# Kernel optimization log

Measured on AMD Instinct MI355X. Metric: run time of the kernel, lower is better.

The kernel has to match this reference:

```python
import jax, jax.numpy as jnp
import numpy as np

HEADS = 16
MAX_SEQ_LEN = 1024
ALPHA = 1.0


def setup_inputs() -> dict:
    key = jax.random.key(0)
    ks = jax.random.split(key, 16)
    b, n, dim = 2, 1024, 1024
    s = 0.02
    x = jax.random.normal(ks[0], (b, n, dim), jnp.float32)
    Wq = jax.random.normal(ks[1], (dim, dim), jnp.float32) * s
    Wk = jax.random.normal(ks[2], (dim, dim), jnp.float32) * s
    Wv = jax.random.normal(ks[3], (dim, dim), jnp.float32) * s
    Wo = jax.random.normal(ks[4], (dim, dim), jnp.float32) * s
    E_idx = jax.random.normal(ks[5], (MAX_SEQ_LEN, HEADS), jnp.float32) * s
    # padding_idx=0 rows zero-initialized (as in torch nn.Embedding(padding_idx=0))
    E_bar = (jax.random.normal(ks[6], (17, HEADS), jnp.float32) * s).at[0].set(0.0)
    E_pos = (jax.random.normal(ks[7], (96, HEADS), jnp.float32) * s).at[0].set(0.0)
    E_oct = (jax.random.normal(ks[8], (25, HEADS), jnp.float32) * s).at[0].set(0.0)
    E_semi = (jax.random.normal(ks[9], (13, HEADS), jnp.float32) * s).at[0].set(0.0)
    # structure matrices: raw values in [0, table_size-2]; forward adds +1
    bar = jax.random.randint(ks[10], (b, n, n), 0, 16, dtype=jnp.int32)
    position = jax.random.randint(ks[11], (b, n, n), 0, 95, dtype=jnp.int32)
    octave = jax.random.randint(ks[12], (b, n, n), 0, 24, dtype=jnp.int32)
    semitone = jax.random.randint(ks[13], (b, n, n), 0, 12, dtype=jnp.int32)
    return {"x": x, "Wq": Wq, "Wk": Wk, "Wv": Wv, "Wo": Wo,
            "E_idx": E_idx, "E_bar": E_bar, "E_pos": E_pos,
            "E_oct": E_oct, "E_semi": E_semi,
            "bar": bar, "position": position, "octave": octave, "semitone": semitone}


def reference(x, Wq, Wk, Wv, Wo, E_idx, E_bar, E_pos, E_oct, E_semi,
              bar, position, octave, semitone):
    b, n, dim = x.shape
    h = HEADS
    d = dim // h

    def split_heads(t):  # (b,n,dim) -> (b,h,n,d)
        return t.reshape(b, n, h, d).transpose(0, 2, 1, 3)

    q = split_heads(x @ Wq.T)
    k = split_heads(x @ Wk.T)
    v = split_heads(x @ Wv.T)

    qk = jnp.einsum('bhid,bhjd->bhij', q, k)

    # relative index bias: (1,h,n,n)
    rel_pos = jnp.clip(jnp.arange(n)[:, None] - jnp.arange(n)[None, :], 0, MAX_SEQ_LEN - 1)
    srel = E_idx[rel_pos].transpose(2, 0, 1)[None]

    # structure biases: embedding lookups -> (b,h,n,n)
    s_time = (E_bar[bar + 1] + E_pos[position + 1]).transpose(0, 3, 1, 2)
    s_pitch = (E_oct[octave + 1] + E_semi[semitone + 1]).transpose(0, 3, 1, 2)

    dots = (qk + ALPHA * (srel + s_time + s_pitch)) / jnp.sqrt(jnp.float32(d))

    causal_mask = jnp.triu(jnp.ones((n, n), dtype=bool), k=1)
    mask_value = -jnp.finfo(dots.dtype).max
    dots = jnp.where(causal_mask, mask_value, dots)

    attn = jax.nn.softmax(dots, axis=-1)  # dropout=0 at eval
    out = jnp.einsum('bhij,bhjd->bhid', attn, v)
    out = out.transpose(0, 2, 1, 3).reshape(b, n, dim)
    return out @ Wo.T
```

## Files before the change

kernel.cpp:

```cpp
#include <hip/hip_runtime.h>
#include <cstdint>
#include <math.h>

typedef __attribute__((ext_vector_type(8))) short short8;
typedef __attribute__((ext_vector_type(4))) float f32x4;

#define LOG2E 1.44269504088896340736f

static __device__ __forceinline__ float bf2f(unsigned short u) {
    union { unsigned int i; float f; } v; v.i = ((unsigned int)u) << 16; return v.f;
}
static __device__ __forceinline__ unsigned short f2bf(float f) {
    union { float f; unsigned int i; } v; v.f = f;
    unsigned int r = v.i + 0x7FFF + ((v.i >> 16) & 1);
    return (unsigned short)(r >> 16);
}

__global__ __launch_bounds__(256) void k_convert(
    const float* __restrict__ x, const float* __restrict__ wq,
    const float* __restrict__ wk, const float* __restrict__ wv,
    const float* __restrict__ wo, unsigned short* __restrict__ dst) {
    long t = (long)blockIdx.x * 256 + threadIdx.x;
    long base = t * 4;
    const long NX = 2097152, NW = 1048576;
    const float* src; long off;
    if (base < NX)            { src = x;  off = base; }
    else if (base < NX + NW)  { src = wq; off = base - NX; }
    else if (base < NX + 2*NW){ src = wk; off = base - NX - NW; }
    else if (base < NX + 3*NW){ src = wv; off = base - NX - 2*NW; }
    else                      { src = wo; off = base - NX - 3*NW; }
    float4 v = *(const float4*)(src + off);
    ushort4 o;
    o.x = f2bf(v.x); o.y = f2bf(v.y); o.z = f2bf(v.z); o.w = f2bf(v.w);
    *(ushort4*)(dst + base) = o;
}

__global__ __launch_bounds__(256) void k_bias(
    const float* __restrict__ Eidx, const float* __restrict__ Ebar,
    const float* __restrict__ Epos, const float* __restrict__ Eoct,
    const float* __restrict__ Esemi,
    const int* __restrict__ barm, const int* __restrict__ posm,
    const int* __restrict__ octm, const int* __restrict__ semim,
    unsigned short* __restrict__ biasg) {
    int fid = blockIdx.x;
    int b = (fid >= 544) ? 1 : 0;
    int f = fid - b * 544;
    int ti, tj;
    if (f >= 480) { int rr = f - 480; ti = 60 + (rr >> 4); tj = rr & 15; }
    else {
        int g = (int)(0.5f * (sqrtf(1.0f + 2.0f * (float)f) - 1.0f));
        while (2 * (g + 1) * (g + 2) <= f) g++;
        while (2 * g * (g + 1) > f) g--;
        int rr = f - 2 * g * (g + 1);
        int q = rr / (g + 1);
        ti = g * 4 + q;
        tj = rr - q * (g + 1);
    }
    int i0 = ti * 16, j0 = tj * 64;

    __shared__ float2 t2[8 * 233];
    __shared__ int    pk[16 * 65];

    int t = threadIdx.x;
    int rel_lo = i0 - j0 - 63; if (rel_lo < 0) rel_lo = 0;

    for (int idx = t; idx < 231 * 8; idx += 256) {
        int s = idx >> 3, h2 = idx & 7;
        float va, vb;
        if (s < 80) {
            int src = rel_lo + s; if (src > 1023) src = 1023;
            va = Eidx[src * 16 + h2]; vb = Eidx[src * 16 + h2 + 8];
        } else if (s < 97)  { va = Ebar[(s - 80) * 16 + h2];  vb = Ebar[(s - 80) * 16 + h2 + 8]; }
        else if (s < 193)   { va = Epos[(s - 97) * 16 + h2];  vb = Epos[(s - 97) * 16 + h2 + 8]; }
        else if (s < 218)   { va = Eoct[(s - 193) * 16 + h2]; vb = Eoct[(s - 193) * 16 + h2 + 8]; }
        else                { va = Esemi[(s - 218) * 16 + h2]; vb = Esemi[(s - 218) * 16 + h2 + 8]; }
        t2[h2 * 233 + s] = make_float2(va, vb);
    }
    #pragma unroll
    for (int cc = 0; cc < 4; cc++) {
        int cell = t + cc * 256;
        int i = i0 + (cell >> 6), j = j0 + (cell & 63);
        long ij = ((long)b << 20) + ((long)i << 10) + j;
        int v = (barm[ij] + 1) | ((posm[ij] + 1) << 5) |
                ((octm[ij] + 1) << 12) | ((semim[ij] + 1) << 17);
        pk[(cell >> 6) * 65 + (cell & 63)] = v;
    }
    __syncthreads();

    int r = t & 15, h2 = (t >> 4) & 7, ah = t >> 7;
    int i = i0 + r;
    int base_rel = i - j0 - rel_lo;
    const float2* T = &t2[h2 * 233];
    long frag = (r >> 2) * 256 + (r & 3) * 4;
    unsigned short* dstL = biasg + ((((long)(b * 16 + h2)     * 64 + ti) * 16 + tj) << 10) + frag;
    unsigned short* dstH = biasg + ((((long)(b * 16 + h2 + 8) * 64 + ti) * 16 + tj) << 10) + frag;
    #pragma unroll 4
    for (int aa = 0; aa < 8; aa++) {
        int a = ah * 8 + aa;
        ushort4 ovL, ovH;
        #pragma unroll
        for (int jj = 0; jj < 4; jj++) {
            int col = a + 16 * jj;
            int p = pk[r * 65 + col];
            int sr = base_rel - col; if (sr < 0) sr = 0;
            float2 v0 = T[sr];
            float2 v1 = T[80  + (p & 31)];
            float2 v2 = T[97  + ((p >> 5)  & 127)];
            float2 v3 = T[193 + ((p >> 12) & 31)];
            float2 v4 = T[218 + ((p >> 17) & 15)];
            float xL = v0.x + v1.x + v2.x + v3.x + v4.x;
            float xH = v0.y + v1.y + v2.y + v3.y + v4.y;
            ((unsigned short*)&ovL)[jj] = f2bf(xL * 0.125f);
            ((unsigned short*)&ovH)[jj] = f2bf(xH * 0.125f);
        }
        *(ushort4*)(dstL + a * 16) = ovL;
        *(ushort4*)(dstH + a * 16) = ovH;
    }
}

__global__ __launch_bounds__(256) void k_gemm(
    const unsigned short* __restrict__ A,
    const unsigned short* __restrict__ B0, const unsigned short* __restrict__ B1,
    const unsigned short* __restrict__ B2,
    unsigned short* __restrict__ qd, unsigned short* __restrict__ kd,
    unsigned short* __restrict__ vtd, float* __restrict__ outf, int mode) {
    __shared__ unsigned short As[128 * 64];
    __shared__ unsigned short Bs[128 * 64];
    int md = (mode < 0) ? (int)blockIdx.z : mode;
    const unsigned short* B = (md == 1) ? B1 : (md == 2) ? B2 : B0;
    int m0 = blockIdx.x * 128, n0 = blockIdx.y * 128;
    int t = threadIdx.x;
    int w = t >> 6, lane = t & 63, g = lane >> 4, c = lane & 15;
    int wr = w >> 1, wc = w & 1;
    const int K = 1024;
    f32x4 zero = {0.f, 0.f, 0.f, 0.f};
    f32x4 acc[4][4];
    #pragma unroll
    for (int m = 0; m < 4; m++)
        #pragma unroll
        for (int n = 0; n < 4; n++) acc[m][n] = zero;

    int srow = w * 8 + (lane >> 3);
    int scol = (lane & 7) * 8;
    for (int k0 = 0; k0 < K; k0 += 64) {
        __syncthreads();
        #pragma unroll
        for (int q = 0; q < 4; q++) {
            int row = q * 32 + srow;
            __builtin_amdgcn_global_load_lds(
                (const __attribute__((address_space(1))) unsigned int*)(A + (long)(m0 + row) * K + k0 + scol),
                (__attribute__((address_space(3))) unsigned int*)&As[(q * 32 + w * 8) * 64],
                16, 0, 0);
            __builtin_amdgcn_global_load_lds(
                (const __attribute__((address_space(1))) unsigned int*)(B + (long)(n0 + row) * K + k0 + scol),
                (__attribute__((address_space(3))) unsigned int*)&Bs[(q * 32 + w * 8) * 64],
                16, 0, 0);
        }
        __syncthreads();
        #pragma unroll
        for (int kk = 0; kk < 2; kk++) {
            short8 a[4], bb[4];
            #pragma unroll
            for (int m = 0; m < 4; m++)
                a[m] = *(const short8*)&As[(wr * 64 + m * 16 + c) * 64 + kk * 32 + g * 8];
            #pragma unroll
            for (int n = 0; n < 4; n++)
                bb[n] = *(const short8*)&Bs[(wc * 64 + n * 16 + c) * 64 + kk * 32 + g * 8];
            #pragma unroll
            for (int m = 0; m < 4; m++)
                #pragma unroll
                for (int n = 0; n < 4; n++)
                    acc[m][n] = __builtin_amdgcn_mfma_f32_16x16x32_bf16(a[m], bb[n], acc[m][n], 0, 0, 0);
        }
    }

    if (md <= 1) {
        unsigned short* dst = (md == 0) ? qd : kd;
        float scale = (md == 0) ? 0.125f : 1.0f;
        #pragma unroll
        for (int m = 0; m < 4; m++) {
            #pragma unroll
            for (int r = 0; r < 4; r++) {
                int mm = m0 + wr * 64 + m * 16 + g * 4 + r;
                int bb2 = mm >> 10, ii = mm & 1023;
                #pragma unroll
                for (int n = 0; n < 4; n++) {
                    int nn = n0 + wc * 64 + n * 16 + c;
                    int hh = nn >> 6, dd = nn & 63;
                    dst[(((long)(bb2 * 16 + hh) << 10) + ii) * 64 + dd] = f2bf(acc[m][n][r] * scale);
                }
            }
        }
    } else if (md == 2) {
        #pragma unroll
        for (int m = 0; m < 4; m++) {
            int mm0 = m0 + wr * 64 + m * 16 + g * 4;
            int bb2 = mm0 >> 10, ii = mm0 & 1023;
            #pragma unroll
            for (int n = 0; n < 4; n++) {
                int nn = n0 + wc * 64 + n * 16 + c;
                int hh = nn >> 6, dd = nn & 63;
                ushort4 pkv;
                pkv.x = f2bf(acc[m][n][0]); pkv.y = f2bf(acc[m][n][1]);
                pkv.z = f2bf(acc[m][n][2]); pkv.w = f2bf(acc[m][n][3]);
                *(ushort4*)&vtd[(((long)(bb2 * 16 + hh) << 6) + dd) * 1024 + ii] = pkv;
            }
        }
    } else {
        #pragma unroll
        for (int m = 0; m < 4; m++) {
            #pragma unroll
            for (int r = 0; r < 4; r++) {
                long mm = m0 + wr * 64 + m * 16 + g * 4 + r;
                #pragma unroll
                for (int n = 0; n < 4; n++) {
                    int nn = n0 + wc * 64 + n * 16 + c;
                    outf[mm * 1024 + nn] = acc[m][n][r];
                }
            }
        }
    }
}

__global__ __launch_bounds__(256) void k_attn(
    const unsigned short* __restrict__ Qs, const unsigned short* __restrict__ Ks,
    const unsigned short* __restrict__ VTs, const unsigned short* __restrict__ biasg,
    unsigned short* __restrict__ Os) {
    __shared__ char smem[4 * 5632];
    int bid = blockIdx.x;
    int it = 63 - (bid >> 5);
    int bh = bid & 31;
    int b = bh >> 4, h = bh & 15;
    int w = threadIdx.x >> 6;
    int lane = threadIdx.x & 63;
    int g = lane >> 4, c = lane & 15;
    int i0 = it * 16;

    char* wbase = smem + w * 5632;
    unsigned short* p_lds = (unsigned short*)wbase;

    long plane = ((long)bh) << 16;
    const unsigned short* Qp = Qs + plane;
    const unsigned short* Kp = Ks + plane;
    const unsigned short* Vp = VTs + plane;
    const unsigned short* Bt = biasg + (((long)bh * 64 + it) << 14);

    short8 q0 = *(const short8*)(Qp + (long)(i0 + c) * 64 + g * 8);
    short8 q1 = *(const short8*)(Qp + (long)(i0 + c) * 64 + 32 + g * 8);

    f32x4 zero = {0.f, 0.f, 0.f, 0.f};
    f32x4 o[4]; o[0] = zero; o[1] = zero; o[2] = zero; o[3] = zero;
    float l[4] = {0.f, 0.f, 0.f, 0.f};

    int nj = (it >> 2) + 1;
    for (int jt = w; jt < nj; jt += 4) {
        int j0 = jt * 64;
        f32x4 s[4]; s[0] = zero; s[1] = zero; s[2] = zero; s[3] = zero;
        #pragma unroll
        for (int jj = 0; jj < 4; jj++) {
            const unsigned short* kr = Kp + (long)(j0 + jj * 16 + c) * 64 + g * 8;
            short8 ka = *(const short8*)(kr);
            short8 kb = *(const short8*)(kr + 32);
            s[jj] = __builtin_amdgcn_mfma_f32_16x16x32_bf16(q0, ka, s[jj], 0, 0, 0);
            s[jj] = __builtin_amdgcn_mfma_f32_16x16x32_bf16(q1, kb, s[jj], 0, 0, 0);
        }
        const unsigned short* bp = Bt + (jt << 10) + lane * 16;
        short8 bv0 = *(const short8*)(bp);
        short8 bv1 = *(const short8*)(bp + 8);
        #pragma unroll
        for (int r = 0; r < 4; r++) {
            #pragma unroll
            for (int jj = 0; jj < 4; jj++) {
                int idx = r * 4 + jj;
                float bb = (idx < 8) ? bf2f((unsigned short)bv0[idx])
                                     : bf2f((unsigned short)bv1[idx - 8]);
                s[jj][r] += bb;
            }
        }
        if (jt == nj - 1) {
            #pragma unroll
            for (int r = 0; r < 4; r++) {
                int i = i0 + g * 4 + r;
                #pragma unroll
                for (int jj = 0; jj < 4; jj++) {
                    if (j0 + jj * 16 + c > i) s[jj][r] = -1e9f;
                }
            }
        }
        #pragma unroll
        for (int r = 0; r < 4; r++) {
            #pragma unroll
            for (int jj = 0; jj < 4; jj++) {
                float p = exp2f(__builtin_fmaf(s[jj][r], LOG2E, -8.0f * LOG2E));
                l[r] += p;
                union { float f; unsigned int u; } pu; pu.f = p;
                p_lds[(g * 4 + r) * 72 + c + 16 * jj] = (unsigned short)(pu.u >> 16);
            }
        }
        short8 pa0 = *(const short8*)&p_lds[c * 72 + g * 8];
        short8 pa1 = *(const short8*)&p_lds[c * 72 + 32 + g * 8];
        #pragma unroll
        for (int dd = 0; dd < 4; dd++) {
            const unsigned short* vb = Vp + (long)(dd * 16 + c) * 1024 + j0 + g * 8;
            short8 v0 = *(const short8*)(vb);
            short8 v1 = *(const short8*)(vb + 32);
            o[dd] = __builtin_amdgcn_mfma_f32_16x16x32_bf16(pa0, v0, o[dd], 0, 0, 0);
            o[dd] = __builtin_amdgcn_mfma_f32_16x16x32_bf16(pa1, v1, o[dd], 0, 0, 0);
        }
    }
    float* oc = (float*)wbase;
    float* lc = (float*)(wbase + 4352);
    #pragma unroll
    for (int dd = 0; dd < 4; dd++)
        #pragma unroll
        for (int r = 0; r < 4; r++)
            oc[lane * 17 + dd * 4 + r] = o[dd][r];
    #pragma unroll
    for (int r = 0; r < 4; r++) lc[lane * 5 + r] = l[r];
    __syncthreads();

    if (w == 0) {
        float linv[4];
        #pragma unroll
        for (int r = 0; r < 4; r++) {
            float lv = 0.f;
            #pragma unroll
            for (int ww = 0; ww < 4; ww++)
                lv += ((const float*)(smem + ww * 5632 + 4352))[lane * 5 + r];
            lv += __shfl_xor(lv, 1); lv += __shfl_xor(lv, 2);
            lv += __shfl_xor(lv, 4); lv += __shfl_xor(lv, 8);
            linv[r] = 1.0f / lv;
        }
        #pragma unroll
        for (int r = 0; r < 4; r++) {
            int i = i0 + g * 4 + r;
            unsigned short* op = Os + ((long)(b * 1024 + i)) * 1024 + h * 64;
            #pragma unroll
            for (int dd = 0; dd < 4; dd++) {
                float ov = 0.f;
                #pragma unroll
                for (int ww = 0; ww < 4; ww++)
                    ov += ((const float*)(smem + ww * 5632))[lane * 17 + dd * 4 + r];
                op[dd * 16 + c] = f2bf(ov * linv[r]);
            }
        }
    }
}

extern "C" void kernel_launch(void* const* d_in, const int* in_sizes, int n_in,
                              void* d_out, int out_size, void* d_ws, size_t ws_size,
                              hipStream_t stream) {
    const float* x     = (const float*)d_in[0];
    const float* Wq    = (const float*)d_in[1];
    const float* Wk    = (const float*)d_in[2];
    const float* Wv    = (const float*)d_in[3];
    const float* Wo    = (const float*)d_in[4];
    const float* Eidx  = (const float*)d_in[5];
    const float* Ebar  = (const float*)d_in[6];
    const float* Epos  = (const float*)d_in[7];
    const float* Eoct  = (const float*)d_in[8];
    const float* Esemi = (const float*)d_in[9];
    const int* barm    = (const int*)d_in[10];
    const int* posm    = (const int*)d_in[11];
    const int* octm    = (const int*)d_in[12];
    const int* semim   = (const int*)d_in[13];
    float* outf = (float*)d_out;

    unsigned short* w = (unsigned short*)d_ws;
    unsigned short* XB   = w;
    unsigned short* WQB  = w + 2097152;
    unsigned short* WKB  = w + 3145728;
    unsigned short* WVB  = w + 4194304;
    unsigned short* WOB  = w + 5242880;
    unsigned short* QS   = w + 6291456;
    unsigned short* KS   = w + 8388608;
    unsigned short* VTS  = w + 10485760;
    unsigned short* OS   = w + 12582912;
    unsigned short* BIAS = w + 14680064;

    k_convert<<<6144, 256, 0, stream>>>(x, Wq, Wk, Wv, Wo, w);
    k_bias<<<1088, 256, 0, stream>>>(Eidx, Ebar, Epos, Eoct, Esemi,
                                     barm, posm, octm, semim, BIAS);
    k_gemm<<<dim3(16, 8, 3), 256, 0, stream>>>(XB, WQB, WKB, WVB,
                                               QS, KS, VTS, nullptr, -1);
    k_attn<<<2048, 256, 0, stream>>>(QS, KS, VTS, BIAS, OS);
    k_gemm<<<dim3(16, 8, 1), 256, 0, stream>>>(OS, WOB, WOB, WOB,
                                               QS, KS, VTS, outf, 3);
}
```

Measured before the change: 119.9 us.

## Widen attention key tile to 128 and split epilogue across waves

Each attention loop iteration now covers 128 keys instead of 64. All K fragments and bias vectors are loaded up front, and the P·V product runs in two 64-key halves, which halves the loop trip count and exposes more memory-level parallelism. The final reduction and output write, previously done only by wave 0, is now spread so each wave handles one row group. The risks are higher register pressure, and worse load balance across the 4 waves for short causal rows, since there are fewer, larger tiles.

Result: slower. 125.0 us (+4.2%).

```diff
diff --git a/kernel.cpp b/kernel.cpp
--- a/kernel.cpp
+++ b/kernel.cpp
@@ -252,29 +252,35 @@
     f32x4 o[4]; o[0] = zero; o[1] = zero; o[2] = zero; o[3] = zero;
     float l[4] = {0.f, 0.f, 0.f, 0.f};
 
-    int nj = (it >> 2) + 1;
+    int nj = (it >> 3) + 1;
     for (int jt = w; jt < nj; jt += 4) {
-        int j0 = jt * 64;
-        f32x4 s[4]; s[0] = zero; s[1] = zero; s[2] = zero; s[3] = zero;
-        #pragma unroll
-        for (int jj = 0; jj < 4; jj++) {
-            const unsigned short* kr = Kp + (long)(j0 + jj * 16 + c) * 64 + g * 8;
-            short8 ka = *(const short8*)(kr);
-            short8 kb = *(const short8*)(kr + 32);
-            s[jj] = __builtin_amdgcn_mfma_f32_16x16x32_bf16(q0, ka, s[jj], 0, 0, 0);
-            s[jj] = __builtin_amdgcn_mfma_f32_16x16x32_bf16(q1, kb, s[jj], 0, 0, 0);
-        }
-        const unsigned short* bp = Bt + (jt << 10) + lane * 16;
-        short8 bv0 = *(const short8*)(bp);
-        short8 bv1 = *(const short8*)(bp + 8);
+        int j0 = jt * 128;
+        short8 ka[8], kb[8];
+        #pragma unroll
+        for (int sub = 0; sub < 8; sub++) {
+            const unsigned short* kr = Kp + (long)(j0 + sub * 16 + c) * 64 + g * 8;
+            ka[sub] = *(const short8*)(kr);
+            kb[sub] = *(const short8*)(kr + 32);
+        }
+        const unsigned short* bp = Bt + (jt << 11) + lane * 16;
+        short8 bv[4];
+        bv[0] = *(const short8*)(bp);
+        bv[1] = *(const short8*)(bp + 8);
+        bv[2] = *(const short8*)(bp + 1024);
+        bv[3] = *(const short8*)(bp + 1032);
+        f32x4 s[8];
+        #pragma unroll
+        for (int sub = 0; sub < 8; sub++) {
+            s[sub] = __builtin_amdgcn_mfma_f32_16x16x32_bf16(q0, ka[sub], zero, 0, 0, 0);
+            s[sub] = __builtin_amdgcn_mfma_f32_16x16x32_bf16(q1, kb[sub], s[sub], 0, 0, 0);
+        }
         #pragma unroll
         for (int r = 0; r < 4; r++) {
             #pragma unroll
-            for (int jj = 0; jj < 4; jj++) {
+            for (int sub = 0; sub < 8; sub++) {
+                int jj = sub & 3, half = sub >> 2;
                 int idx = r * 4 + jj;
-                float bb = (idx < 8) ? bf2f((unsigned short)bv0[idx])
-                                     : bf2f((unsigned short)bv1[idx - 8]);
-                s[jj][r] += bb;
+                s[sub][r] += bf2f((unsigned short)bv[half * 2 + (idx >> 3)][idx & 7]);
             }
         }
         if (jt == nj - 1) {
@@ -282,30 +288,38 @@
             for (int r = 0; r < 4; r++) {
                 int i = i0 + g * 4 + r;
                 #pragma unroll
-                for (int jj = 0; jj < 4; jj++) {
-                    if (j0 + jj * 16 + c > i) s[jj][r] = -1e9f;
-                }
+                for (int sub = 0; sub < 8; sub++)
+                    if (j0 + sub * 16 + c > i) s[sub][r] = -1e9f;
             }
         }
         #pragma unroll
         for (int r = 0; r < 4; r++) {
             #pragma unroll
-            for (int jj = 0; jj < 4; jj++) {
-                float p = exp2f(__builtin_fmaf(s[jj][r], LOG2E, -8.0f * LOG2E));
+            for (int sub = 0; sub < 8; sub++) {
+                float p = exp2f(__builtin_fmaf(s[sub][r], LOG2E, -8.0f * LOG2E));
                 l[r] += p;
                 union { float f; unsigned int u; } pu; pu.f = p;
-                p_lds[(g * 4 + r) * 72 + c + 16 * jj] = (unsigned short)(pu.u >> 16);
-            }
-        }
-        short8 pa0 = *(const short8*)&p_lds[c * 72 + g * 8];
-        short8 pa1 = *(const short8*)&p_lds[c * 72 + 32 + g * 8];
-        #pragma unroll
-        for (int dd = 0; dd < 4; dd++) {
-            const unsigned short* vb = Vp + (long)(dd * 16 + c) * 1024 + j0 + g * 8;
-            short8 v0 = *(const short8*)(vb);
-            short8 v1 = *(const short8*)(vb + 32);
-            o[dd] = __builtin_amdgcn_mfma_f32_16x16x32_bf16(pa0, v0, o[dd], 0, 0, 0);
-            o[dd] = __builtin_amdgcn_mfma_f32_16x16x32_bf16(pa1, v1, o[dd], 0, 0, 0);
+                p_lds[(g * 4 + r) * 136 + sub * 16 + c] = (unsigned short)(pu.u >> 16);
+            }
+        }
+        short8 pa[4];
+        #pragma unroll
+        for (int ch = 0; ch < 4; ch++)
+            pa[ch] = *(const short8*)&p_lds[c * 136 + ch * 32 + g * 8];
+        #pragma unroll
+        for (int half = 0; half < 2; half++) {
+            short8 v0[4], v1[4];
+            #pragma unroll
+            for (int dd = 0; dd < 4; dd++) {
+                const unsigned short* vb = Vp + (long)(dd * 16 + c) * 1024 + j0 + half * 64 + g * 8;
+                v0[dd] = *(const short8*)(vb);
+                v1[dd] = *(const short8*)(vb + 32);
+            }
+            #pragma unroll
+            for (int dd = 0; dd < 4; dd++) {
+                o[dd] = __builtin_amdgcn_mfma_f32_16x16x32_bf16(pa[half * 2],     v0[dd], o[dd], 0, 0, 0);
+                o[dd] = __builtin_amdgcn_mfma_f32_16x16x32_bf16(pa[half * 2 + 1], v1[dd], o[dd], 0, 0, 0);
+            }
         }
     }
     float* oc = (float*)wbase;
@@ -319,30 +333,24 @@
     for (int r = 0; r < 4; r++) lc[lane * 5 + r] = l[r];
     __syncthreads();
 
-    if (w == 0) {
-        float linv[4];
-        #pragma unroll
-        for (int r = 0; r < 4; r++) {
-            float lv = 0.f;
+    {
+        int r = w;
+        float lv = 0.f;
+        #pragma unroll
+        for (int ww = 0; ww < 4; ww++)
+            lv += ((const float*)(smem + ww * 5632 + 4352))[lane * 5 + r];
+        lv += __shfl_xor(lv, 1); lv += __shfl_xor(lv, 2);
+        lv += __shfl_xor(lv, 4); lv += __shfl_xor(lv, 8);
+        float linv = 1.0f / lv;
+        int i = i0 + g * 4 + r;
+        unsigned short* op = Os + ((long)(b * 1024 + i)) * 1024 + h * 64;
+        #pragma unroll
+        for (int dd = 0; dd < 4; dd++) {
+            float ov = 0.f;
             #pragma unroll
             for (int ww = 0; ww < 4; ww++)
-                lv += ((const float*)(smem + ww * 5632 + 4352))[lane * 5 + r];
-            lv += __shfl_xor(lv, 1); lv += __shfl_xor(lv, 2);
-            lv += __shfl_xor(lv, 4); lv += __shfl_xor(lv, 8);
-            linv[r] = 1.0f / lv;
-        }
-        #pragma unroll
-        for (int r = 0; r < 4; r++) {
-            int i = i0 + g * 4 + r;
-            unsigned short* op = Os + ((long)(b * 1024 + i)) * 1024 + h * 64;
-            #pragma unroll
-            for (int dd = 0; dd < 4; dd++) {
-                float ov = 0.f;
-                #pragma unroll
-                for (int ww = 0; ww < 4; ww++)
-                    ov += ((const float*)(smem + ww * 5632))[lane * 17 + dd * 4 + r];
-                op[dd * 16 + c] = f2bf(ov * linv[r]);
-            }
+                ov += ((const float*)(smem + ww * 5632))[lane * 17 + dd * 4 + r];
+            op[dd * 16 + c] = f2bf(ov * linv);
         }
     }
 }
```
